# Kernel optimization log

Hardware: AMD Instinct MI355X
Metric: run time of the kernel (lower is better)

## Reference

```python
import jax, jax.numpy as jnp
import numpy as np

D_EQUI, D_INV, D_MSG, N_HEADS, D_FF = 64, 256, 64, 8, 256
D_EDGE_IN, D_EDGE_OUT = 64, 64
D_OUT = D_EQUI + N_HEADS + D_EDGE_OUT  # 136
IN_FEATS = 2 * D_MSG + D_EQUI + D_EDGE_IN  # 256
B, N = 4, 256
NEG_INF = -1e9  # finite stand-in for -inf in adj_to_attn_mask


def setup_inputs() -> dict:
    key = jax.random.key(0)
    ks = jax.random.split(key, 20)
    def rn(k, shape, scale):
        return jax.random.normal(k, shape, dtype=jnp.float32) * scale
    inp = {
        "equis": rn(ks[0], (B, N, 3, D_EQUI), 1.0),
        "invs": rn(ks[1], (B, N, D_INV), 1.0),
        "edges": rn(ks[2], (B, N, N, D_EDGE_IN), 1.0),
        "adj_matrix": jax.random.randint(ks[3], (B, N, N), 0, 2, dtype=jnp.int32),
        # _PairwiseMessages params
        "Wq": rn(ks[4], (D_MSG, D_INV), D_INV ** -0.5),
        "bq": jnp.zeros((D_MSG,), jnp.float32),
        "Wk": rn(ks[5], (D_MSG, D_INV), D_INV ** -0.5),
        "bk": jnp.zeros((D_MSG,), jnp.float32),
        "W1": rn(ks[6], (D_FF, IN_FEATS), IN_FEATS ** -0.5),
        "b1": jnp.zeros((D_FF,), jnp.float32),
        "W2": rn(ks[7], (D_OUT, D_FF), D_FF ** -0.5),
        "b2": jnp.zeros((D_OUT,), jnp.float32),
        # _EquiAttention params (no bias)
        "Wc": rn(ks[8], (D_EQUI, D_EQUI), D_EQUI ** -0.5),
        "Wa": rn(ks[9], (D_EQUI, D_EQUI), D_EQUI ** -0.5),
        # _InvAttention params
        "Wi": rn(ks[10], (D_INV, D_INV), D_INV ** -0.5),
        "bi": jnp.zeros((D_INV,), jnp.float32),
        "Wo": rn(ks[11], (D_INV, D_INV), D_INV ** -0.5),
        "bo": jnp.zeros((D_INV,), jnp.float32),
    }
    return inp


def _forward(equis, invs, edges, adj_matrix, Wq, bq, Wk, bk, W1, b1, W2, b2, Wc, Wa, Wi, bi, Wo, bo):
    # ---- _PairwiseMessages ----
    # per-channel dot products over the 3 coordinates: [B, Nq, Nk, d_equi]
    dotprods = jnp.einsum("bqcd,bkcd->bqkd", equis, equis)
    q_msg = invs @ Wq.T + bq          # [B, N, d_msg]
    k_msg = invs @ Wk.T + bk          # [B, N, d_msg]
    Nq = invs.shape[1]
    pairwise = jnp.concatenate(
        (
            jnp.broadcast_to(q_msg[:, :, None, :], (B, Nq, Nq, D_MSG)),
            jnp.broadcast_to(k_msg[:, None, :, :], (B, Nq, Nq, D_MSG)),
            dotprods,
            edges,
        ),
        axis=-1,
    )  # [B, Nq, Nk, in_feats]
    h = jax.nn.silu(pairwise @ W1.T + b1)
    messages = h @ W2.T + b2          # [B, Nq, Nk, d_out]

    equi_msg = messages[..., :D_EQUI]
    inv_msg = messages[..., D_EQUI : D_EQUI + N_HEADS]
    edge_out = messages[..., D_EQUI + N_HEADS :]

    attn_mask = jnp.where(adj_matrix > 0, 0.0, NEG_INF).astype(equi_msg.dtype)  # [B,Nq,Nk]

    # ---- _EquiAttention ----
    attn_e = jax.nn.softmax(equi_msg + attn_mask[..., None], axis=2)  # [B,Nq,Nk,d_equi]
    proj_equi = equis @ Wc.T                                          # [B,Nk,3,d_equi]
    attn_out_e = jnp.einsum("bqkd,bkcd->bqcd", attn_e, proj_equi)     # [B,Nq,3,d_equi]
    w_e = jnp.sqrt(jnp.sum(attn_e ** 2, axis=2))                      # [B,Nq,d_equi]
    attn_out_e = attn_out_e * w_e[:, :, None, :]
    equi_updates = attn_out_e @ Wa.T

    # ---- _InvAttention ----
    attn_i = jax.nn.softmax(inv_msg + attn_mask[..., None], axis=2)   # [B,Nq,Nk,H]
    proj_feats = invs @ Wi.T + bi                                     # [B,Nk,d_inv]
    head_feats = proj_feats.reshape(B, Nq, N_HEADS, D_INV // N_HEADS)
    attn_out_i = jnp.einsum("bqkh,bkhd->bqhd", attn_i, head_feats)    # [B,Nq,H,d_head]
    w_i = jnp.sqrt(jnp.sum(attn_i ** 2, axis=2))                      # [B,Nq,H]
    attn_out_i = attn_out_i * w_i[..., None]
    inv_updates = attn_out_i.reshape(B, Nq, D_INV) @ Wo.T + bo

    return equi_updates, inv_updates, edge_out


def reference(equis, invs, edges, adj_matrix, Wq, bq, Wk, bk, W1, b1, W2, b2, Wc, Wa, Wi, bi, Wo, bo):
    return _forward(equis, invs, edges, adj_matrix, Wq, bq, Wk, bk, W1, b1, W2, b2, Wc, Wa, Wi, bi, Wo, bo)
```

## Files before the change

### kernel.cpp

```cpp
#include <hip/hip_runtime.h>
#include <hip/hip_bf16.h>
#include <cstdint>


typedef __bf16 bf16x8_t __attribute__((ext_vector_type(8)));
typedef float  f32x4_t  __attribute__((ext_vector_type(4)));

#define SP 76
#define KV 32

__device__ __forceinline__ int swzX(int row, int col) {
    return row * 192 + (col ^ ((row & 7) << 3));
}
__device__ __forceinline__ int swzH(int row, int col) {
    return (row << 8) + (col ^ ((row & 7) << 3));
}

__device__ __forceinline__ bf16x8_t cvt8(f32x4_t a, f32x4_t b) {
    bf16x8_t r;
    r[0] = (__bf16)a.x; r[1] = (__bf16)a.y; r[2] = (__bf16)a.z; r[3] = (__bf16)a.w;
    r[4] = (__bf16)b.x; r[5] = (__bf16)b.y; r[6] = (__bf16)b.z; r[7] = (__bf16)b.w;
    return r;
}

__global__ __launch_bounds__(256) void semla_pre(
    const float* __restrict__ invs, const float* __restrict__ equis,
    const float* __restrict__ Wq, const float* __restrict__ bq,
    const float* __restrict__ Wk, const float* __restrict__ bk,
    const float* __restrict__ Wc, const float* __restrict__ Wi, const float* __restrict__ bi,
    const float* __restrict__ W1, const float* __restrict__ W2,
    __bf16* __restrict__ W1bf, __bf16* __restrict__ W2bf,
    float* __restrict__ qc, float* __restrict__ kmsg,
    float* __restrict__ pTE, float* __restrict__ pTF)
{
    const int blk = blockIdx.x, tid = threadIdx.x;
    if (blk < 256) {
        const int r0 = blk * 4;
        __shared__ __align__(16) float sInv4[4][256];
        __shared__ __align__(16) float sEqu4[4][192];
        __shared__ __align__(16) float sQm4[4][64];
        #pragma unroll
        for (int j = 0; j < 4; ++j) {
            sInv4[j][tid] = invs[(size_t)(r0 + j) * 256 + tid];
            if (tid < 192) sEqu4[j][tid] = equis[(size_t)(r0 + j) * 192 + tid];
        }
        __syncthreads();
        {
            float acc[4] = {0.f, 0.f, 0.f, 0.f};
            const float* w = &Wi[tid * 256];
            for (int i = 0; i < 256; i += 4) {
                f32x4_t ww = *(const f32x4_t*)&w[i];
                #pragma unroll
                for (int j = 0; j < 4; ++j) {
                    const float* x = &sInv4[j][i];
                    acc[j] += ww.x * x[0] + ww.y * x[1] + ww.z * x[2] + ww.w * x[3];
                }
            }
            const float bb = bi[tid];
            #pragma unroll
            for (int j = 0; j < 4; ++j) {
                const int bb_ = (r0 + j) >> 8, nl = (r0 + j) & 255;
                pTF[((size_t)bb_ * 256 + tid) * 256 + nl] = acc[j] + bb;
            }
        }
        if (tid < 128) {
            const int d = tid & 63;
            const float* w = (tid < 64) ? &Wq[d * 256] : &Wk[d * 256];
            float acc[4] = {0.f, 0.f, 0.f, 0.f};
            for (int i = 0; i < 256; i += 4) {
                f32x4_t ww = *(const f32x4_t*)&w[i];
                #pragma unroll
                for (int j = 0; j < 4; ++j) {
                    const float* x = &sInv4[j][i];
                    acc[j] += ww.x * x[0] + ww.y * x[1] + ww.z * x[2] + ww.w * x[3];
                }
            }
            if (tid < 64) {
                const float bb = bq[d];
                #pragma unroll
                for (int j = 0; j < 4; ++j) sQm4[j][d] = acc[j] + bb;
            } else {
                const float bb = bk[d];
                #pragma unroll
                for (int j = 0; j < 4; ++j) kmsg[(size_t)(r0 + j) * 64 + d] = acc[j] + bb;
            }
        }
        if (tid < 192) {
            const int c = tid >> 6, e = tid & 63;
            const float* w = &Wc[e * 64];
            float acc[4] = {0.f, 0.f, 0.f, 0.f};
            for (int dd = 0; dd < 64; dd += 4) {
                f32x4_t ww = *(const f32x4_t*)&w[dd];
                #pragma unroll
                for (int j = 0; j < 4; ++j) {
                    const float* x = &sEqu4[j][c * 64 + dd];
                    acc[j] += ww.x * x[0] + ww.y * x[1] + ww.z * x[2] + ww.w * x[3];
                }
            }
            #pragma unroll
            for (int j = 0; j < 4; ++j) {
                const int bb_ = (r0 + j) >> 8, nl = (r0 + j) & 255;
                pTE[(((size_t)bb_ * 3 + c) * 64 + e) * 256 + nl] = acc[j];
            }
        }
        __syncthreads();
        {
            const float* w = &W1[tid * 256];
            float acc[4] = {0.f, 0.f, 0.f, 0.f};
            for (int d = 0; d < 64; d += 4) {
                f32x4_t ww = *(const f32x4_t*)&w[d];
                #pragma unroll
                for (int j = 0; j < 4; ++j) {
                    const float* x = &sQm4[j][d];
                    acc[j] += ww.x * x[0] + ww.y * x[1] + ww.z * x[2] + ww.w * x[3];
                }
            }
            #pragma unroll
            for (int j = 0; j < 4; ++j) qc[(size_t)(r0 + j) * 256 + tid] = acc[j];
        }
    } else if (blk < 268) {
        const int base = (blk - 256) * 4096;
        #pragma unroll
        for (int it = 0; it < 16; ++it) {
            const int e = base + it * 256 + tid;
            const int o = e / 192, k = e % 192;
            W1bf[e] = (__bf16)W1[o * 256 + 64 + k];
        }
    } else if (blk < 277) {
        const int base = (blk - 268) * 4096;
        #pragma unroll
        for (int it = 0; it < 16; ++it) {
            const int e = base + it * 256 + tid;
            const int o = e >> 8, cc = e & 255;
            const int src = (o < 64) ? (72 + o) : (o < 136 ? o - 64 : -1);
            W2bf[e] = (src >= 0) ? (__bf16)W2[src * 256 + cc] : (__bf16)0.f;
        }
    }
}

__global__ __launch_bounds__(512, 2) void semla_main(
    const float* __restrict__ equis, const float* __restrict__ edges,
    const int* __restrict__ adj,
    const __bf16* __restrict__ W1bf, const __bf16* __restrict__ W2bf,
    const float* __restrict__ qc, const float* __restrict__ kmsg,
    const float* __restrict__ pTE, const float* __restrict__ pTF,
    const float* __restrict__ b1, const float* __restrict__ b2,
    float* __restrict__ outE, float* __restrict__ outI, float* __restrict__ outEdge)
{
    const int bqid = ((blockIdx.x & 7) << 7) | (blockIdx.x >> 3);
    const int b = bqid >> 8;
    const int tid = threadIdx.x;
    const int wave = tid >> 6, lane = tid & 63;
    const int arow = lane & 15, kgrp = lane >> 4;

    __shared__ __align__(16) __bf16 sX[KV * 192];
    __shared__ __align__(16) __bf16 sH[KV * 256];
    __shared__ __align__(16) float  sS[KV * SP];
    __shared__ __align__(16) float  sB1[256];
    __shared__ __align__(16) float  sB2[144];
    __shared__ __align__(16) float  sEquiQ[192];
    __shared__ float sF[72], sL[72], sL2[72];
    __shared__ int   sAdj[KV];

    if (tid < 256) sB1[tid] = b1[tid] + qc[(size_t)bqid * 256 + tid];
    if (tid < 144) sB2[tid] = (tid < 64) ? b2[72 + tid] : (tid < 136 ? b2[tid - 64] : 0.f);
    if (tid < 192) sEquiQ[tid] = equis[(size_t)bqid * 192 + tid];

    bf16x8_t w1r[6][2];
    #pragma unroll
    for (int ks = 0; ks < 6; ++ks)
        #pragma unroll
        for (int cf = 0; cf < 2; ++cf)
            w1r[ks][cf] = *(const bf16x8_t*)
                &W1bf[((wave << 5) + (cf << 4) + arow) * 192 + ks * 32 + (kgrp << 3)];
    bf16x8_t w2r[8], w2r2[8];
    #pragma unroll
    for (int ks = 0; ks < 8; ++ks)
        w2r[ks] = *(const bf16x8_t*)
            &W2bf[(((wave << 4) + arow) << 8) + ks * 32 + (kgrp << 3)];
    if (wave == 7) {
        #pragma unroll
        for (int ks = 0; ks < 8; ++ks)
            w2r2[ks] = *(const bf16x8_t*)
                &W2bf[((128 + arow) << 8) + ks * 32 + (kgrp << 3)];
    }

    float m_run = -1e30f, l_run = 0.f, l2_run = 0.f;
    float m_rn2 = -1e30f, l_rn2 = 0.f, l2_rn2 = 0.f;
    float accE = 0.f;
    float accI = 0.f;
    const int c_e = tid >> 6, d_e = tid & 63;
    const int fidx = tid - 256, h_i = (tid - 256) >> 5;

    __syncthreads();

    for (int kt = 0; kt < 8; ++kt) {
        const int k0 = kt * KV;
        const int kb = b * 256 + k0;

        #pragma unroll
        for (int gi = 0; gi < 2; ++gi) {
            const int g = (gi == 0) ? tid : 512 + tid;
            if (gi == 1 && tid >= 256) continue;
            const int row = g / 24, c8 = (g % 24) << 3;
            if (c8 < 64) {
                const float* p = &kmsg[(size_t)(kb + row) * 64 + c8];
                *(bf16x8_t*)&sX[swzX(row, c8)] =
                    cvt8(*(const f32x4_t*)p, *(const f32x4_t*)(p + 4));
            } else if (c8 < 128) {
                const int d0 = c8 - 64;
                const float* ek = &equis[(size_t)(kb + row) * 192 + d0];
                f32x4_t e0a = *(const f32x4_t*)(ek),       e0b = *(const f32x4_t*)(ek + 4);
                f32x4_t e1a = *(const f32x4_t*)(ek + 64),  e1b = *(const f32x4_t*)(ek + 68);
                f32x4_t e2a = *(const f32x4_t*)(ek + 128), e2b = *(const f32x4_t*)(ek + 132);
                f32x4_t q0a = *(const f32x4_t*)&sEquiQ[d0],       q0b = *(const f32x4_t*)&sEquiQ[d0 + 4];
                f32x4_t q1a = *(const f32x4_t*)&sEquiQ[64 + d0],  q1b = *(const f32x4_t*)&sEquiQ[68 + d0];
                f32x4_t q2a = *(const f32x4_t*)&sEquiQ[128 + d0], q2b = *(const f32x4_t*)&sEquiQ[132 + d0];
                *(bf16x8_t*)&sX[swzX(row, c8)] =
                    cvt8(e0a * q0a + e1a * q1a + e2a * q2a,
                         e0b * q0b + e1b * q1b + e2b * q2b);
            } else {
                const float* p = &edges[((size_t)bqid * 256 + k0 + row) * 64 + (c8 - 128)];
                *(bf16x8_t*)&sX[swzX(row, c8)] =
                    cvt8(*(const f32x4_t*)p, *(const f32x4_t*)(p + 4));
            }
        }
        if (tid < KV) sAdj[tid] = adj[(size_t)bqid * 256 + k0 + tid];
        if (kt > 0) {
            const int k0P = k0 - KV;
            if (tid < 192) {
                float a = accE * sF[d_e];
                const float* pe = &pTE[(((size_t)b * 3 + c_e) * 64 + d_e) * 256 + k0P];
                #pragma unroll
                for (int t = 0; t < 8; ++t) {
                    f32x4_t w = *(const f32x4_t*)&pe[t * 4];
                    a += sS[(4 * t + 0) * SP + d_e] * w.x;
                    a += sS[(4 * t + 1) * SP + d_e] * w.y;
                    a += sS[(4 * t + 2) * SP + d_e] * w.z;
                    a += sS[(4 * t + 3) * SP + d_e] * w.w;
                }
                accE = a;
            }
            if (tid >= 256) {
                float a = accI * sF[64 + h_i];
                const float* pf = &pTF[((size_t)b * 256 + fidx) * 256 + k0P];
                #pragma unroll
                for (int t = 0; t < 8; ++t) {
                    f32x4_t w = *(const f32x4_t*)&pf[t * 4];
                    a += sS[(4 * t + 0) * SP + 64 + h_i] * w.x;
                    a += sS[(4 * t + 1) * SP + 64 + h_i] * w.y;
                    a += sS[(4 * t + 2) * SP + 64 + h_i] * w.z;
                    a += sS[(4 * t + 3) * SP + 64 + h_i] * w.w;
                }
                accI = a;
            }
        }
        __syncthreads();

        f32x4_t acc1[2][2];
        {
            const f32x4_t z = {0.f, 0.f, 0.f, 0.f};
            acc1[0][0] = z; acc1[0][1] = z; acc1[1][0] = z; acc1[1][1] = z;
        }
        #pragma unroll
        for (int ks = 0; ks < 6; ++ks) {
            const int kk = ks * 32 + (kgrp << 3);
            bf16x8_t a0 = *(const bf16x8_t*)&sX[swzX(arow, kk)];
            bf16x8_t a1 = *(const bf16x8_t*)&sX[swzX(16 + arow, kk)];
            acc1[0][0] = __builtin_amdgcn_mfma_f32_16x16x32_bf16(a0, w1r[ks][0], acc1[0][0], 0, 0, 0);
            acc1[0][1] = __builtin_amdgcn_mfma_f32_16x16x32_bf16(a0, w1r[ks][1], acc1[0][1], 0, 0, 0);
            acc1[1][0] = __builtin_amdgcn_mfma_f32_16x16x32_bf16(a1, w1r[ks][0], acc1[1][0], 0, 0, 0);
            acc1[1][1] = __builtin_amdgcn_mfma_f32_16x16x32_bf16(a1, w1r[ks][1], acc1[1][1], 0, 0, 0);
        }
        #pragma unroll
        for (int rt = 0; rt < 2; ++rt)
            #pragma unroll
            for (int cf = 0; cf < 2; ++cf) {
                const int ccol = (wave << 5) + (cf << 4) + arow;
                const float bb = sB1[ccol];
                #pragma unroll
                for (int j = 0; j < 4; ++j) {
                    const int row = (rt << 4) + (kgrp << 2) + j;
                    float x = acc1[rt][cf][j] + bb;
                    sH[swzH(row, ccol)] = (__bf16)(x / (1.f + __expf(-x)));
                }
            }
        __syncthreads();

        f32x4_t acc2[2], acc2b[2];
        {
            const f32x4_t z = {0.f, 0.f, 0.f, 0.f};
            acc2[0] = z; acc2[1] = z; acc2b[0] = z; acc2b[1] = z;
        }
        #pragma unroll
        for (int ks = 0; ks < 8; ++ks) {
            const int kk = ks * 32 + (kgrp << 3);
            bf16x8_t a0 = *(const bf16x8_t*)&sH[swzH(arow, kk)];
            bf16x8_t a1 = *(const bf16x8_t*)&sH[swzH(16 + arow, kk)];
            acc2[0] = __builtin_amdgcn_mfma_f32_16x16x32_bf16(a0, w2r[ks], acc2[0], 0, 0, 0);
            acc2[1] = __builtin_amdgcn_mfma_f32_16x16x32_bf16(a1, w2r[ks], acc2[1], 0, 0, 0);
            if (wave == 7) {
                acc2b[0] = __builtin_amdgcn_mfma_f32_16x16x32_bf16(a0, w2r2[ks], acc2b[0], 0, 0, 0);
                acc2b[1] = __builtin_amdgcn_mfma_f32_16x16x32_bf16(a1, w2r2[ks], acc2b[1], 0, 0, 0);
            }
        }
        const int col = (wave << 4) + arow;
        if (wave < 4) {
            const float bb2 = sB2[col];
            #pragma unroll
            for (int rt = 0; rt < 2; ++rt)
                #pragma unroll
                for (int j = 0; j < 4; ++j) {
                    const int r = (rt << 4) + (kgrp << 2) + j;
                    outEdge[((size_t)bqid * 256 + k0 + r) * 64 + col] = acc2[rt][j] + bb2;
                }
        } else {
            const int ch = col - 64;
            const float bb2 = sB2[col];
            float s_[8]; int ad_[8];
            float xm = -1e30f;
            #pragma unroll
            for (int rt = 0; rt < 2; ++rt)
                #pragma unroll
                for (int j = 0; j < 4; ++j) {
                    const int r = (rt << 4) + (kgrp << 2) + j;
                    const float v = acc2[rt][j] + bb2;
                    s_[rt * 4 + j] = v;
                    ad_[rt * 4 + j] = sAdj[r];
                    if (ad_[rt * 4 + j]) xm = fmaxf(xm, v);
                }
            xm = fmaxf(xm, __shfl_xor(xm, 16));
            xm = fmaxf(xm, __shfl_xor(xm, 32));
            const float mN = fmaxf(m_run, xm);
            const float f = __expf(m_run - mN);
            float s1 = 0.f, s2 = 0.f;
            #pragma unroll
            for (int rt = 0; rt < 2; ++rt)
                #pragma unroll
                for (int j = 0; j < 4; ++j) {
                    const int r = (rt << 4) + (kgrp << 2) + j;
                    const float p = ad_[rt * 4 + j] ? __expf(s_[rt * 4 + j] - mN) : 0.f;
                    sS[r * SP + ch] = p;
                    s1 += p; s2 += p * p;
                }
            s1 += __shfl_xor(s1, 16); s1 += __shfl_xor(s1, 32);
            s2 += __shfl_xor(s2, 16); s2 += __shfl_xor(s2, 32);
            l_run = l_run * f + s1;
            l2_run = l2_run * f * f + s2;
            m_run = mN;
            if (kgrp == 0) sF[ch] = f;
        }
        if (wave == 7) {
            const float bb3 = sB2[128 + (arow & 7)];
            float s_[8]; int ad_[8];
            float xm = -1e30f;
            #pragma unroll
            for (int rt = 0; rt < 2; ++rt)
                #pragma unroll
                for (int j = 0; j < 4; ++j) {
                    const int r = (rt << 4) + (kgrp << 2) + j;
                    const float v = acc2b[rt][j] + bb3;
                    s_[rt * 4 + j] = v;
                    ad_[rt * 4 + j] = sAdj[r];
                    if (ad_[rt * 4 + j]) xm = fmaxf(xm, v);
                }
            xm = fmaxf(xm, __shfl_xor(xm, 16));
            xm = fmaxf(xm, __shfl_xor(xm, 32));
            const float mN = fmaxf(m_rn2, xm);
            const float f = __expf(m_rn2 - mN);
            float s1 = 0.f, s2 = 0.f;
            #pragma unroll
            for (int rt = 0; rt < 2; ++rt)
                #pragma unroll
                for (int j = 0; j < 4; ++j) {
                    const int r = (rt << 4) + (kgrp << 2) + j;
                    const float p = ad_[rt * 4 + j] ? __expf(s_[rt * 4 + j] - mN) : 0.f;
                    if (arow < 8) sS[r * SP + 64 + arow] = p;
                    s1 += p; s2 += p * p;
                }
            s1 += __shfl_xor(s1, 16); s1 += __shfl_xor(s1, 32);
            s2 += __shfl_xor(s2, 16); s2 += __shfl_xor(s2, 32);
            l_rn2 = l_rn2 * f + s1;
            l2_rn2 = l2_rn2 * f * f + s2;
            m_rn2 = mN;
            if (kgrp == 0 && arow < 8) sF[64 + arow] = f;
        }
        __syncthreads();
    }

    {
        const int k0P = 224;
        if (tid < 192) {
            float a = accE * sF[d_e];
            const float* pe = &pTE[(((size_t)b * 3 + c_e) * 64 + d_e) * 256 + k0P];
            #pragma unroll
            for (int t = 0; t < 8; ++t) {
                f32x4_t w = *(const f32x4_t*)&pe[t * 4];
                a += sS[(4 * t + 0) * SP + d_e] * w.x;
                a += sS[(4 * t + 1) * SP + d_e] * w.y;
                a += sS[(4 * t + 2) * SP + d_e] * w.z;
                a += sS[(4 * t + 3) * SP + d_e] * w.w;
            }
            accE = a;
        }
        if (tid >= 256) {
            float a = accI * sF[64 + h_i];
            const float* pf = &pTF[((size_t)b * 256 + fidx) * 256 + k0P];
            #pragma unroll
            for (int t = 0; t < 8; ++t) {
                f32x4_t w = *(const f32x4_t*)&pf[t * 4];
                a += sS[(4 * t + 0) * SP + 64 + h_i] * w.x;
                a += sS[(4 * t + 1) * SP + 64 + h_i] * w.y;
                a += sS[(4 * t + 2) * SP + 64 + h_i] * w.z;
                a += sS[(4 * t + 3) * SP + 64 + h_i] * w.w;
            }
            accI = a;
        }
    }

    if (wave >= 4 && kgrp == 0) {
        const int ch = ((wave - 4) << 4) + arow;
        sL[ch] = l_run; sL2[ch] = l2_run;
        if (wave == 7 && arow < 8) { sL[64 + arow] = l_rn2; sL2[64 + arow] = l2_rn2; }
    }
    __syncthreads();
    if (tid < 192) {
        const float ll = sL[d_e];
        outE[(size_t)bqid * 192 + tid] = accE * sqrtf(sL2[d_e]) / (ll * ll);
    }
    if (tid >= 256) {
        const float ll = sL[64 + h_i];
        outI[(size_t)bqid * 256 + fidx] = accI * sqrtf(sL2[64 + h_i]) / (ll * ll);
    }
}

__global__ __launch_bounds__(256) void semla_post(
    const float* __restrict__ Wa, const float* __restrict__ Wo,
    const float* __restrict__ bo,
    float* __restrict__ outE, float* __restrict__ outI)
{
    __shared__ __align__(16) float hE[4][192];
    __shared__ __align__(16) float hI[4][256];
    const int blk = blockIdx.x, tid = threadIdx.x;
    const int r0 = blk * 4;
    #pragma unroll
    for (int r = 0; r < 4; ++r) {
        if (tid < 192) hE[r][tid] = outE[(size_t)(r0 + r) * 192 + tid];
        hI[r][tid] = outI[(size_t)(r0 + r) * 256 + tid];
    }
    __syncthreads();
    if (tid < 192) {
        const int c = tid >> 6, e = tid & 63;
        float wa[64];
        #pragma unroll
        for (int d = 0; d < 64; d += 4) {
            f32x4_t w = *(const f32x4_t*)&Wa[e * 64 + d];
            wa[d] = w.x; wa[d + 1] = w.y; wa[d + 2] = w.z; wa[d + 3] = w.w;
        }
        #pragma unroll
        for (int r = 0; r < 4; ++r) {
            float s = 0.f;
            #pragma unroll
            for (int d = 0; d < 64; ++d) s += hE[r][c * 64 + d] * wa[d];
            outE[((size_t)(r0 + r) * 3 + c) * 64 + e] = s;
        }
    }
    {
        const float bb = bo[tid];
        const float* wo = &Wo[tid * 256];
        #pragma unroll
        for (int r = 0; r < 4; ++r) {
            float s = 0.f;
            for (int i = 0; i < 256; i += 4) {
                f32x4_t w = *(const f32x4_t*)&wo[i];
                s += w.x * hI[r][i] + w.y * hI[r][i + 1]
                   + w.z * hI[r][i + 2] + w.w * hI[r][i + 3];
            }
            outI[(size_t)(r0 + r) * 256 + tid] = s + bb;
        }
    }
}

extern "C" void kernel_launch(void* const* d_in, const int* in_sizes, int n_in,
                              void* d_out, int out_size, void* d_ws, size_t ws_size,
                              hipStream_t stream) {
    (void)in_sizes; (void)n_in; (void)out_size; (void)ws_size;
    const float* equis = (const float*)d_in[0];
    const float* invs  = (const float*)d_in[1];
    const float* edges = (const float*)d_in[2];
    const int*   adj   = (const int*)d_in[3];
    const float* Wq = (const float*)d_in[4];
    const float* bq = (const float*)d_in[5];
    const float* Wk = (const float*)d_in[6];
    const float* bk = (const float*)d_in[7];
    const float* W1 = (const float*)d_in[8];
    const float* b1 = (const float*)d_in[9];
    const float* W2 = (const float*)d_in[10];
    const float* b2 = (const float*)d_in[11];
    const float* Wc = (const float*)d_in[12];
    const float* Wa = (const float*)d_in[13];
    const float* Wi = (const float*)d_in[14];
    const float* bi = (const float*)d_in[15];
    const float* Wo = (const float*)d_in[16];
    const float* bo = (const float*)d_in[17];

    float* out = (float*)d_out;
    float* outE    = out;
    float* outI    = out + 196608;
    float* outEdge = out + 458752;

    char* ws = (char*)d_ws;
    __bf16* W1bf = (__bf16*)(ws);
    __bf16* W2bf = (__bf16*)(ws + 98304);
    float* qc    = (float*)(ws + 172032);
    float* kmsg  = (float*)(ws + 1220608);
    float* pTE   = (float*)(ws + 1482752);
    float* pTF   = (float*)(ws + 2269184);

    semla_pre<<<277, 256, 0, stream>>>(invs, equis, Wq, bq, Wk, bk, Wc, Wi, bi,
                                       W1, W2, W1bf, W2bf, qc, kmsg, pTE, pTF);
    semla_main<<<1024, 512, 0, stream>>>(equis, edges, adj, W1bf, W2bf, qc, kmsg,
                                         pTE, pTF, b1, b2,
                                         outE, outI, outEdge);
    semla_post<<<256, 256, 0, stream>>>(Wa, Wo, bo, outE, outI);
}
```

Before: 299.5 us.

## Software-pipeline next K-tile loads into registers and drop a barrier per iteration

Moves the global loads for the next key tile (kmsg, equis dot-product inputs, edges, adjacency) into registers issued before the GEMM and softmax stages, then writes them to shared memory at the end of the iteration. The first tile is staged before the loop, adjacency is double-buffered, and one __syncthreads per iteration is removed. The aim is to hide global-memory latency behind MFMA work, at the cost of higher register pressure, which may reduce occupancy.

```diff
diff --git a/kernel.cpp b/kernel.cpp
--- a/kernel.cpp
+++ b/kernel.cpp
@@ -3,6 +3,7 @@
 #include <cstdint>
 
 
+typedef __bf16 bf16x4_t __attribute__((ext_vector_type(4)));
 typedef __bf16 bf16x8_t __attribute__((ext_vector_type(8)));
 typedef float  f32x4_t  __attribute__((ext_vector_type(4)));
 
@@ -20,6 +21,11 @@
     bf16x8_t r;
     r[0] = (__bf16)a.x; r[1] = (__bf16)a.y; r[2] = (__bf16)a.z; r[3] = (__bf16)a.w;
     r[4] = (__bf16)b.x; r[5] = (__bf16)b.y; r[6] = (__bf16)b.z; r[7] = (__bf16)b.w;
+    return r;
+}
+__device__ __forceinline__ bf16x4_t cvt4(f32x4_t a) {
+    bf16x4_t r;
+    r[0] = (__bf16)a.x; r[1] = (__bf16)a.y; r[2] = (__bf16)a.z; r[3] = (__bf16)a.w;
     return r;
 }
 
@@ -160,7 +166,7 @@
     __shared__ __align__(16) float  sB2[144];
     __shared__ __align__(16) float  sEquiQ[192];
     __shared__ float sF[72], sL[72], sL2[72];
-    __shared__ int   sAdj[KV];
+    __shared__ int   sAdj[2][KV];
 
     if (tid < 256) sB1[tid] = b1[tid] + qc[(size_t)bqid * 256 + tid];
     if (tid < 144) sB2[tid] = (tid < 64) ? b2[72 + tid] : (tid < 136 ? b2[tid - 64] : 0.f);
@@ -192,40 +198,45 @@
     const int c_e = tid >> 6, d_e = tid & 63;
     const int fidx = tid - 256, h_i = (tid - 256) >> 5;
 
+    const int rowS = (tid & 255) >> 3;
+    const int c8S = (tid & 7) << 3;
+    const int pchunk = tid >> 1, prow = pchunk >> 3;
+    const int pcol = 128 + ((pchunk & 7) << 3) + ((tid & 1) << 2);
+
+    __syncthreads();
+
+    {
+        if (tid < 256) {
+            const float* p = &kmsg[(size_t)(b * 256 + rowS) * 64 + c8S];
+            *(bf16x8_t*)&sX[swzX(rowS, c8S)] =
+                cvt8(*(const f32x4_t*)p, *(const f32x4_t*)(p + 4));
+        } else {
+            const float* ek = &equis[(size_t)(b * 256 + rowS) * 192 + c8S];
+            f32x4_t e0a = *(const f32x4_t*)(ek),       e0b = *(const f32x4_t*)(ek + 4);
+            f32x4_t e1a = *(const f32x4_t*)(ek + 64),  e1b = *(const f32x4_t*)(ek + 68);
+            f32x4_t e2a = *(const f32x4_t*)(ek + 128), e2b = *(const f32x4_t*)(ek + 132);
+            f32x4_t q0a = *(const f32x4_t*)&sEquiQ[c8S],       q0b = *(const f32x4_t*)&sEquiQ[c8S + 4];
+            f32x4_t q1a = *(const f32x4_t*)&sEquiQ[64 + c8S],  q1b = *(const f32x4_t*)&sEquiQ[68 + c8S];
+            f32x4_t q2a = *(const f32x4_t*)&sEquiQ[128 + c8S], q2b = *(const f32x4_t*)&sEquiQ[132 + c8S];
+            *(bf16x8_t*)&sX[swzX(rowS, 64 + c8S)] =
+                cvt8(e0a * q0a + e1a * q1a + e2a * q2a,
+                     e0b * q0b + e1b * q1b + e2b * q2b);
+        }
+        f32x4_t ed = *(const f32x4_t*)&edges[((size_t)bqid * 256 + prow) * 64 + (pcol - 128)];
+        *(bf16x4_t*)&sX[swzX(prow, pcol)] = cvt4(ed);
+        if (tid < KV) sAdj[0][tid] = adj[(size_t)bqid * 256 + tid];
+    }
     __syncthreads();
 
     for (int kt = 0; kt < 8; ++kt) {
         const int k0 = kt * KV;
-        const int kb = b * 256 + k0;
-
-        #pragma unroll
-        for (int gi = 0; gi < 2; ++gi) {
-            const int g = (gi == 0) ? tid : 512 + tid;
-            if (gi == 1 && tid >= 256) continue;
-            const int row = g / 24, c8 = (g % 24) << 3;
-            if (c8 < 64) {
-                const float* p = &kmsg[(size_t)(kb + row) * 64 + c8];
-                *(bf16x8_t*)&sX[swzX(row, c8)] =
-                    cvt8(*(const f32x4_t*)p, *(const f32x4_t*)(p + 4));
-            } else if (c8 < 128) {
-                const int d0 = c8 - 64;
-                const float* ek = &equis[(size_t)(kb + row) * 192 + d0];
-                f32x4_t e0a = *(const f32x4_t*)(ek),       e0b = *(const f32x4_t*)(ek + 4);
-                f32x4_t e1a = *(const f32x4_t*)(ek + 64),  e1b = *(const f32x4_t*)(ek + 68);
-                f32x4_t e2a = *(const f32x4_t*)(ek + 128), e2b = *(const f32x4_t*)(ek + 132);
-                f32x4_t q0a = *(const f32x4_t*)&sEquiQ[d0],       q0b = *(const f32x4_t*)&sEquiQ[d0 + 4];
-                f32x4_t q1a = *(const f32x4_t*)&sEquiQ[64 + d0],  q1b = *(const f32x4_t*)&sEquiQ[68 + d0];
-                f32x4_t q2a = *(const f32x4_t*)&sEquiQ[128 + d0], q2b = *(const f32x4_t*)&sEquiQ[132 + d0];
-                *(bf16x8_t*)&sX[swzX(row, c8)] =
-                    cvt8(e0a * q0a + e1a * q1a + e2a * q2a,
-                         e0b * q0b + e1b * q1b + e2b * q2b);
-            } else {
-                const float* p = &edges[((size_t)bqid * 256 + k0 + row) * 64 + (c8 - 128)];
-                *(bf16x8_t*)&sX[swzX(row, c8)] =
-                    cvt8(*(const f32x4_t*)p, *(const f32x4_t*)(p + 4));
-            }
-        }
-        if (tid < KV) sAdj[tid] = adj[(size_t)bqid * 256 + k0 + tid];
+        const int cur = kt & 1;
+
+        f32x4_t edPf = {0.f, 0.f, 0.f, 0.f};
+        if (kt < 7)
+            edPf = *(const f32x4_t*)
+                &edges[((size_t)bqid * 256 + k0 + KV + prow) * 64 + (pcol - 128)];
+
         if (kt > 0) {
             const int k0P = k0 - KV;
             if (tid < 192) {
@@ -255,7 +266,6 @@
                 accI = a;
             }
         }
-        __syncthreads();
 
         f32x4_t acc1[2][2];
         {
@@ -286,6 +296,24 @@
                 }
             }
         __syncthreads();
+
+        f32x4_t kmA, kmB;
+        f32x4_t e0a_, e0b_, e1a_, e1b_, e2a_, e2b_;
+        int adjN = 0;
+        if (kt < 7) {
+            const int kbN = b * 256 + k0 + KV;
+            if (tid < 256) {
+                const float* p = &kmsg[(size_t)(kbN + rowS) * 64 + c8S];
+                kmA = *(const f32x4_t*)p;
+                kmB = *(const f32x4_t*)(p + 4);
+            } else {
+                const float* ek = &equis[(size_t)(kbN + rowS) * 192 + c8S];
+                e0a_ = *(const f32x4_t*)(ek);       e0b_ = *(const f32x4_t*)(ek + 4);
+                e1a_ = *(const f32x4_t*)(ek + 64);  e1b_ = *(const f32x4_t*)(ek + 68);
+                e2a_ = *(const f32x4_t*)(ek + 128); e2b_ = *(const f32x4_t*)(ek + 132);
+            }
+            if (tid < KV) adjN = adj[(size_t)bqid * 256 + k0 + KV + tid];
+        }
 
         f32x4_t acc2[2], acc2b[2];
         {
@@ -326,7 +354,7 @@
                     const int r = (rt << 4) + (kgrp << 2) + j;
                     const float v = acc2[rt][j] + bb2;
                     s_[rt * 4 + j] = v;
-                    ad_[rt * 4 + j] = sAdj[r];
+                    ad_[rt * 4 + j] = sAdj[cur][r];
                     if (ad_[rt * 4 + j]) xm = fmaxf(xm, v);
                 }
             xm = fmaxf(xm, __shfl_xor(xm, 16));
@@ -361,7 +389,7 @@
                     const int r = (rt << 4) + (kgrp << 2) + j;
                     const float v = acc2b[rt][j] + bb3;
                     s_[rt * 4 + j] = v;
-                    ad_[rt * 4 + j] = sAdj[r];
+                    ad_[rt * 4 + j] = sAdj[cur][r];
                     if (ad_[rt * 4 + j]) xm = fmaxf(xm, v);
                 }
             xm = fmaxf(xm, __shfl_xor(xm, 16));
@@ -384,6 +412,21 @@
             l2_rn2 = l2_rn2 * f * f + s2;
             m_rn2 = mN;
             if (kgrp == 0 && arow < 8) sF[64 + arow] = f;
+        }
+
+        if (kt < 7) {
+            if (tid < 256) {
+                *(bf16x8_t*)&sX[swzX(rowS, c8S)] = cvt8(kmA, kmB);
+            } else {
+                f32x4_t q0a = *(const f32x4_t*)&sEquiQ[c8S],       q0b = *(const f32x4_t*)&sEquiQ[c8S + 4];
+                f32x4_t q1a = *(const f32x4_t*)&sEquiQ[64 + c8S],  q1b = *(const f32x4_t*)&sEquiQ[68 + c8S];
+                f32x4_t q2a = *(const f32x4_t*)&sEquiQ[128 + c8S], q2b = *(const f32x4_t*)&sEquiQ[132 + c8S];
+                *(bf16x8_t*)&sX[swzX(rowS, 64 + c8S)] =
+                    cvt8(e0a_ * q0a + e1a_ * q1a + e2a_ * q2a,
+                         e0b_ * q0b + e1b_ * q1b + e2b_ * q2b);
+            }
+            *(bf16x4_t*)&sX[swzX(prow, pcol)] = cvt4(edPf);
+            if (tid < KV) sAdj[cur ^ 1][tid] = adjN;
         }
         __syncthreads();
     }
```

New measurement: 299.0 us. About the same (-0.2%).

## Enlarge key tile to 128 and store transposed bf16 attention weights

Applied to the files above, without the earlier changes.

Raises the key tile from 32 to 128, so the main loop runs 2 iterations instead of 8. Each wave now computes 8 row tiles of the two MFMA GEMMs per iteration, and staging of the second tile is interleaved with the attention-weighted accumulation of the first. Softmax probabilities are stored transposed as bf16 and read back as 8-wide vectors. The extra-head work moves to wave 3. The aim is fewer barriers and better reuse of register-resident weights, at the cost of much larger register and LDS footprints (risk of spills and lower occupancy) and reduced precision of the probabilities.

```diff
diff --git a/kernel.cpp b/kernel.cpp
--- a/kernel.cpp
+++ b/kernel.cpp
@@ -6,8 +6,8 @@
 typedef __bf16 bf16x8_t __attribute__((ext_vector_type(8)));
 typedef float  f32x4_t  __attribute__((ext_vector_type(4)));
 
-#define SP 76
-#define KV 32
+#define KV 128
+#define PP 144
 
 __device__ __forceinline__ int swzX(int row, int col) {
     return row * 192 + (col ^ ((row & 7) << 3));
@@ -155,7 +155,7 @@
 
     __shared__ __align__(16) __bf16 sX[KV * 192];
     __shared__ __align__(16) __bf16 sH[KV * 256];
-    __shared__ __align__(16) float  sS[KV * SP];
+    __shared__ __align__(16) __bf16 sSt[72 * PP];
     __shared__ __align__(16) float  sB1[256];
     __shared__ __align__(16) float  sB2[144];
     __shared__ __align__(16) float  sEquiQ[192];
@@ -173,17 +173,15 @@
         for (int cf = 0; cf < 2; ++cf)
             w1r[ks][cf] = *(const bf16x8_t*)
                 &W1bf[((wave << 5) + (cf << 4) + arow) * 192 + ks * 32 + (kgrp << 3)];
-    bf16x8_t w2r[8], w2r2[8];
+    bf16x8_t w2r[8];
     #pragma unroll
     for (int ks = 0; ks < 8; ++ks)
         w2r[ks] = *(const bf16x8_t*)
             &W2bf[(((wave << 4) + arow) << 8) + ks * 32 + (kgrp << 3)];
-    if (wave == 7) {
-        #pragma unroll
-        for (int ks = 0; ks < 8; ++ks)
-            w2r2[ks] = *(const bf16x8_t*)
-                &W2bf[((128 + arow) << 8) + ks * 32 + (kgrp << 3)];
-    }
+    bf16x8_t w2r2[8];
+    #pragma unroll
+    for (int ks = 0; ks < 8; ++ks)
+        w2r2[ks] = *(const bf16x8_t*)&W2bf[((128 + arow) << 8) + ks * 32 + (kgrp << 3)];
 
     float m_run = -1e30f, l_run = 0.f, l2_run = 0.f;
     float m_rn2 = -1e30f, l_rn2 = 0.f, l2_rn2 = 0.f;
@@ -192,123 +190,109 @@
     const int c_e = tid >> 6, d_e = tid & 63;
     const int fidx = tid - 256, h_i = (tid - 256) >> 5;
 
+    const int rowT = tid >> 2, sub = tid & 3;
+
     __syncthreads();
 
-    for (int kt = 0; kt < 8; ++kt) {
-        const int k0 = kt * KV;
-        const int kb = b * 256 + k0;
-
-        #pragma unroll
-        for (int gi = 0; gi < 2; ++gi) {
-            const int g = (gi == 0) ? tid : 512 + tid;
-            if (gi == 1 && tid >= 256) continue;
-            const int row = g / 24, c8 = (g % 24) << 3;
-            if (c8 < 64) {
-                const float* p = &kmsg[(size_t)(kb + row) * 64 + c8];
-                *(bf16x8_t*)&sX[swzX(row, c8)] =
+    auto STAGE = [&](int kt) {
+        const int k0s = kt * KV;
+        const int kbs = b * 256 + k0s;
+        #pragma unroll
+        for (int ci = 0; ci < 6; ++ci) {
+            const int cc = sub + ci * 4;
+            const int c0 = cc << 3;
+            if (cc < 8) {
+                const float* p = &kmsg[(size_t)(kbs + rowT) * 64 + c0];
+                *(bf16x8_t*)&sX[swzX(rowT, c0)] =
                     cvt8(*(const f32x4_t*)p, *(const f32x4_t*)(p + 4));
-            } else if (c8 < 128) {
-                const int d0 = c8 - 64;
-                const float* ek = &equis[(size_t)(kb + row) * 192 + d0];
+            } else if (cc < 16) {
+                const int d0 = c0 - 64;
+                const float* ek = &equis[(size_t)(kbs + rowT) * 192 + d0];
                 f32x4_t e0a = *(const f32x4_t*)(ek),       e0b = *(const f32x4_t*)(ek + 4);
                 f32x4_t e1a = *(const f32x4_t*)(ek + 64),  e1b = *(const f32x4_t*)(ek + 68);
                 f32x4_t e2a = *(const f32x4_t*)(ek + 128), e2b = *(const f32x4_t*)(ek + 132);
                 f32x4_t q0a = *(const f32x4_t*)&sEquiQ[d0],       q0b = *(const f32x4_t*)&sEquiQ[d0 + 4];
                 f32x4_t q1a = *(const f32x4_t*)&sEquiQ[64 + d0],  q1b = *(const f32x4_t*)&sEquiQ[68 + d0];
                 f32x4_t q2a = *(const f32x4_t*)&sEquiQ[128 + d0], q2b = *(const f32x4_t*)&sEquiQ[132 + d0];
-                *(bf16x8_t*)&sX[swzX(row, c8)] =
+                *(bf16x8_t*)&sX[swzX(rowT, c0)] =
                     cvt8(e0a * q0a + e1a * q1a + e2a * q2a,
                          e0b * q0b + e1b * q1b + e2b * q2b);
             } else {
-                const float* p = &edges[((size_t)bqid * 256 + k0 + row) * 64 + (c8 - 128)];
-                *(bf16x8_t*)&sX[swzX(row, c8)] =
+                const float* p = &edges[((size_t)bqid * 256 + k0s + rowT) * 64 + (c0 - 128)];
+                *(bf16x8_t*)&sX[swzX(rowT, c0)] =
                     cvt8(*(const f32x4_t*)p, *(const f32x4_t*)(p + 4));
             }
         }
-        if (tid < KV) sAdj[tid] = adj[(size_t)bqid * 256 + k0 + tid];
-        if (kt > 0) {
-            const int k0P = k0 - KV;
-            if (tid < 192) {
-                float a = accE * sF[d_e];
-                const float* pe = &pTE[(((size_t)b * 3 + c_e) * 64 + d_e) * 256 + k0P];
-                #pragma unroll
-                for (int t = 0; t < 8; ++t) {
-                    f32x4_t w = *(const f32x4_t*)&pe[t * 4];
-                    a += sS[(4 * t + 0) * SP + d_e] * w.x;
-                    a += sS[(4 * t + 1) * SP + d_e] * w.y;
-                    a += sS[(4 * t + 2) * SP + d_e] * w.z;
-                    a += sS[(4 * t + 3) * SP + d_e] * w.w;
-                }
-                accE = a;
-            }
-            if (tid >= 256) {
-                float a = accI * sF[64 + h_i];
-                const float* pf = &pTF[((size_t)b * 256 + fidx) * 256 + k0P];
-                #pragma unroll
-                for (int t = 0; t < 8; ++t) {
-                    f32x4_t w = *(const f32x4_t*)&pf[t * 4];
-                    a += sS[(4 * t + 0) * SP + 64 + h_i] * w.x;
-                    a += sS[(4 * t + 1) * SP + 64 + h_i] * w.y;
-                    a += sS[(4 * t + 2) * SP + 64 + h_i] * w.z;
-                    a += sS[(4 * t + 3) * SP + 64 + h_i] * w.w;
-                }
-                accI = a;
-            }
-        }
-        __syncthreads();
-
-        f32x4_t acc1[2][2];
+        if (tid < KV) sAdj[tid] = adj[(size_t)bqid * 256 + k0s + tid];
+    };
+
+    STAGE(0);
+    __syncthreads();
+
+    for (int kt = 0; kt < 2; ++kt) {
+        const int k0 = kt * KV;
+
+        f32x4_t acc1[8][2];
         {
             const f32x4_t z = {0.f, 0.f, 0.f, 0.f};
-            acc1[0][0] = z; acc1[0][1] = z; acc1[1][0] = z; acc1[1][1] = z;
+            #pragma unroll
+            for (int rt = 0; rt < 8; ++rt) { acc1[rt][0] = z; acc1[rt][1] = z; }
         }
         #pragma unroll
         for (int ks = 0; ks < 6; ++ks) {
             const int kk = ks * 32 + (kgrp << 3);
-            bf16x8_t a0 = *(const bf16x8_t*)&sX[swzX(arow, kk)];
-            bf16x8_t a1 = *(const bf16x8_t*)&sX[swzX(16 + arow, kk)];
-            acc1[0][0] = __builtin_amdgcn_mfma_f32_16x16x32_bf16(a0, w1r[ks][0], acc1[0][0], 0, 0, 0);
-            acc1[0][1] = __builtin_amdgcn_mfma_f32_16x16x32_bf16(a0, w1r[ks][1], acc1[0][1], 0, 0, 0);
-            acc1[1][0] = __builtin_amdgcn_mfma_f32_16x16x32_bf16(a1, w1r[ks][0], acc1[1][0], 0, 0, 0);
-            acc1[1][1] = __builtin_amdgcn_mfma_f32_16x16x32_bf16(a1, w1r[ks][1], acc1[1][1], 0, 0, 0);
-        }
-        #pragma unroll
-        for (int rt = 0; rt < 2; ++rt)
-            #pragma unroll
-            for (int cf = 0; cf < 2; ++cf) {
-                const int ccol = (wave << 5) + (cf << 4) + arow;
-                const float bb = sB1[ccol];
+            bf16x8_t a[8];
+            #pragma unroll
+            for (int rt = 0; rt < 8; ++rt)
+                a[rt] = *(const bf16x8_t*)&sX[swzX((rt << 4) + arow, kk)];
+            #pragma unroll
+            for (int rt = 0; rt < 8; ++rt) {
+                acc1[rt][0] = __builtin_amdgcn_mfma_f32_16x16x32_bf16(a[rt], w1r[ks][0], acc1[rt][0], 0, 0, 0);
+                acc1[rt][1] = __builtin_amdgcn_mfma_f32_16x16x32_bf16(a[rt], w1r[ks][1], acc1[rt][1], 0, 0, 0);
+            }
+        }
+        #pragma unroll
+        for (int cf = 0; cf < 2; ++cf) {
+            const int ccol = (wave << 5) + (cf << 4) + arow;
+            const float bb = sB1[ccol];
+            #pragma unroll
+            for (int rt = 0; rt < 8; ++rt)
                 #pragma unroll
                 for (int j = 0; j < 4; ++j) {
                     const int row = (rt << 4) + (kgrp << 2) + j;
                     float x = acc1[rt][cf][j] + bb;
                     sH[swzH(row, ccol)] = (__bf16)(x / (1.f + __expf(-x)));
                 }
-            }
+        }
         __syncthreads();
 
-        f32x4_t acc2[2], acc2b[2];
+        f32x4_t acc2[8], acc2b[8];
         {
             const f32x4_t z = {0.f, 0.f, 0.f, 0.f};
-            acc2[0] = z; acc2[1] = z; acc2b[0] = z; acc2b[1] = z;
+            #pragma unroll
+            for (int rt = 0; rt < 8; ++rt) { acc2[rt] = z; acc2b[rt] = z; }
         }
         #pragma unroll
         for (int ks = 0; ks < 8; ++ks) {
             const int kk = ks * 32 + (kgrp << 3);
-            bf16x8_t a0 = *(const bf16x8_t*)&sH[swzH(arow, kk)];
-            bf16x8_t a1 = *(const bf16x8_t*)&sH[swzH(16 + arow, kk)];
-            acc2[0] = __builtin_amdgcn_mfma_f32_16x16x32_bf16(a0, w2r[ks], acc2[0], 0, 0, 0);
-            acc2[1] = __builtin_amdgcn_mfma_f32_16x16x32_bf16(a1, w2r[ks], acc2[1], 0, 0, 0);
-            if (wave == 7) {
-                acc2b[0] = __builtin_amdgcn_mfma_f32_16x16x32_bf16(a0, w2r2[ks], acc2b[0], 0, 0, 0);
-                acc2b[1] = __builtin_amdgcn_mfma_f32_16x16x32_bf16(a1, w2r2[ks], acc2b[1], 0, 0, 0);
+            bf16x8_t a[8];
+            #pragma unroll
+            for (int rt = 0; rt < 8; ++rt)
+                a[rt] = *(const bf16x8_t*)&sH[swzH((rt << 4) + arow, kk)];
+            #pragma unroll
+            for (int rt = 0; rt < 8; ++rt)
+                acc2[rt] = __builtin_amdgcn_mfma_f32_16x16x32_bf16(a[rt], w2r[ks], acc2[rt], 0, 0, 0);
+            if (wave == 3) {
+                #pragma unroll
+                for (int rt = 0; rt < 8; ++rt)
+                    acc2b[rt] = __builtin_amdgcn_mfma_f32_16x16x32_bf16(a[rt], w2r2[ks], acc2b[rt], 0, 0, 0);
             }
         }
         const int col = (wave << 4) + arow;
         if (wave < 4) {
             const float bb2 = sB2[col];
             #pragma unroll
-            for (int rt = 0; rt < 2; ++rt)
+            for (int rt = 0; rt < 8; ++rt)
                 #pragma unroll
                 for (int j = 0; j < 4; ++j) {
                     const int r = (rt << 4) + (kgrp << 2) + j;
@@ -317,17 +301,17 @@
         } else {
             const int ch = col - 64;
             const float bb2 = sB2[col];
-            float s_[8]; int ad_[8];
+            float s_[32];
+            unsigned adm = 0;
             float xm = -1e30f;
             #pragma unroll
-            for (int rt = 0; rt < 2; ++rt)
+            for (int rt = 0; rt < 8; ++rt)
                 #pragma unroll
                 for (int j = 0; j < 4; ++j) {
                     const int r = (rt << 4) + (kgrp << 2) + j;
                     const float v = acc2[rt][j] + bb2;
                     s_[rt * 4 + j] = v;
-                    ad_[rt * 4 + j] = sAdj[r];
-                    if (ad_[rt * 4 + j]) xm = fmaxf(xm, v);
+                    if (sAdj[r]) { adm |= (1u << (rt * 4 + j)); xm = fmaxf(xm, v); }
                 }
             xm = fmaxf(xm, __shfl_xor(xm, 16));
             xm = fmaxf(xm, __shfl_xor(xm, 32));
@@ -335,12 +319,13 @@
             const float f = __expf(m_run - mN);
             float s1 = 0.f, s2 = 0.f;
             #pragma unroll
-            for (int rt = 0; rt < 2; ++rt)
+            for (int rt = 0; rt < 8; ++rt)
                 #pragma unroll
                 for (int j = 0; j < 4; ++j) {
                     const int r = (rt << 4) + (kgrp << 2) + j;
-                    const float p = ad_[rt * 4 + j] ? __expf(s_[rt * 4 + j] - mN) : 0.f;
-                    sS[r * SP + ch] = p;
+                    const float p = ((adm >> (rt * 4 + j)) & 1u)
+                                    ? __expf(s_[rt * 4 + j] - mN) : 0.f;
+                    sSt[ch * PP + r] = (__bf16)p;
                     s1 += p; s2 += p * p;
                 }
             s1 += __shfl_xor(s1, 16); s1 += __shfl_xor(s1, 32);
@@ -350,19 +335,19 @@
             m_run = mN;
             if (kgrp == 0) sF[ch] = f;
         }
-        if (wave == 7) {
+        if (wave == 3) {
             const float bb3 = sB2[128 + (arow & 7)];
-            float s_[8]; int ad_[8];
+            float s_[32];
+            unsigned adm = 0;
             float xm = -1e30f;
             #pragma unroll
-            for (int rt = 0; rt < 2; ++rt)
+            for (int rt = 0; rt < 8; ++rt)
                 #pragma unroll
                 for (int j = 0; j < 4; ++j) {
                     const int r = (rt << 4) + (kgrp << 2) + j;
                     const float v = acc2b[rt][j] + bb3;
                     s_[rt * 4 + j] = v;
-                    ad_[rt * 4 + j] = sAdj[r];
-                    if (ad_[rt * 4 + j]) xm = fmaxf(xm, v);
+                    if (sAdj[r]) { adm |= (1u << (rt * 4 + j)); xm = fmaxf(xm, v); }
                 }
             xm = fmaxf(xm, __shfl_xor(xm, 16));
             xm = fmaxf(xm, __shfl_xor(xm, 32));
@@ -370,12 +355,13 @@
             const float f = __expf(m_rn2 - mN);
             float s1 = 0.f, s2 = 0.f;
             #pragma unroll
-            for (int rt = 0; rt < 2; ++rt)
+            for (int rt = 0; rt < 8; ++rt)
                 #pragma unroll
                 for (int j = 0; j < 4; ++j) {
                     const int r = (rt << 4) + (kgrp << 2) + j;
-                    const float p = ad_[rt * 4 + j] ? __expf(s_[rt * 4 + j] - mN) : 0.f;
-                    if (arow < 8) sS[r * SP + 64 + arow] = p;
+                    const float p = ((adm >> (rt * 4 + j)) & 1u)
+                                    ? __expf(s_[rt * 4 + j] - mN) : 0.f;
+                    if (arow < 8) sSt[(64 + arow) * PP + r] = (__bf16)p;
                     s1 += p; s2 += p * p;
                 }
             s1 += __shfl_xor(s1, 16); s1 += __shfl_xor(s1, 32);
@@ -386,43 +372,48 @@
             if (kgrp == 0 && arow < 8) sF[64 + arow] = f;
         }
         __syncthreads();
-    }
-
-    {
-        const int k0P = 224;
+
+        if (kt == 0) STAGE(1);
         if (tid < 192) {
             float a = accE * sF[d_e];
-            const float* pe = &pTE[(((size_t)b * 3 + c_e) * 64 + d_e) * 256 + k0P];
-            #pragma unroll
-            for (int t = 0; t < 8; ++t) {
-                f32x4_t w = *(const f32x4_t*)&pe[t * 4];
-                a += sS[(4 * t + 0) * SP + d_e] * w.x;
-                a += sS[(4 * t + 1) * SP + d_e] * w.y;
-                a += sS[(4 * t + 2) * SP + d_e] * w.z;
-                a += sS[(4 * t + 3) * SP + d_e] * w.w;
+            const float* pe = &pTE[(((size_t)b * 3 + c_e) * 64 + d_e) * 256 + k0];
+            const __bf16* ps = &sSt[d_e * PP];
+            #pragma unroll
+            for (int t = 0; t < 16; ++t) {
+                bf16x8_t pv = *(const bf16x8_t*)&ps[t * 8];
+                f32x4_t w0 = *(const f32x4_t*)&pe[t * 8];
+                f32x4_t w1 = *(const f32x4_t*)&pe[t * 8 + 4];
+                a += (float)pv[0] * w0.x + (float)pv[1] * w0.y
+                   + (float)pv[2] * w0.z + (float)pv[3] * w0.w
+                   + (float)pv[4] * w1.x + (float)pv[5] * w1.y
+                   + (float)pv[6] * w1.z + (float)pv[7] * w1.w;
             }
             accE = a;
         }
         if (tid >= 256) {
             float a = accI * sF[64 + h_i];
-            const float* pf = &pTF[((size_t)b * 256 + fidx) * 256 + k0P];
-            #pragma unroll
-            for (int t = 0; t < 8; ++t) {
-                f32x4_t w = *(const f32x4_t*)&pf[t * 4];
-                a += sS[(4 * t + 0) * SP + 64 + h_i] * w.x;
-                a += sS[(4 * t + 1) * SP + 64 + h_i] * w.y;
-                a += sS[(4 * t + 2) * SP + 64 + h_i] * w.z;
-                a += sS[(4 * t + 3) * SP + 64 + h_i] * w.w;
+            const float* pf = &pTF[((size_t)b * 256 + fidx) * 256 + k0];
+            const __bf16* ps = &sSt[(64 + h_i) * PP];
+            #pragma unroll
+            for (int t = 0; t < 16; ++t) {
+                bf16x8_t pv = *(const bf16x8_t*)&ps[t * 8];
+                f32x4_t w0 = *(const f32x4_t*)&pf[t * 8];
+                f32x4_t w1 = *(const f32x4_t*)&pf[t * 8 + 4];
+                a += (float)pv[0] * w0.x + (float)pv[1] * w0.y
+                   + (float)pv[2] * w0.z + (float)pv[3] * w0.w
+                   + (float)pv[4] * w1.x + (float)pv[5] * w1.y
+                   + (float)pv[6] * w1.z + (float)pv[7] * w1.w;
             }
             accI = a;
         }
+        __syncthreads();
     }
 
     if (wave >= 4 && kgrp == 0) {
         const int ch = ((wave - 4) << 4) + arow;
         sL[ch] = l_run; sL2[ch] = l2_run;
-        if (wave == 7 && arow < 8) { sL[64 + arow] = l_rn2; sL2[64 + arow] = l2_rn2; }
-    }
+    }
+    if (wave == 3 && kgrp == 0 && arow < 8) { sL[64 + arow] = l_rn2; sL2[64 + arow] = l2_rn2; }
     __syncthreads();
     if (tid < 192) {
         const float ll = sL[d_e];
```

New measurement: 516.7 us. +72.5%, slower.
